# Kernel tuning notes

Measured on AMD Instinct MI355X. Metric: run time of the kernel, lower is better.

## Reference

```python
import jax, jax.numpy as jnp
import numpy as np


def setup_inputs() -> dict:
    key = jax.random.key(0)
    ks = jax.random.split(key, 8)
    B = 32768
    return {
        "x": jax.random.normal(ks[0], (B, 784), dtype=jnp.float32),
        "conv_w": jax.random.normal(ks[1], (3, 3), dtype=jnp.float32),
        "fc1_w": jax.random.normal(ks[2], (512, 676), dtype=jnp.float32) * 0.04,
        "fc1_b": jax.random.normal(ks[3], (512,), dtype=jnp.float32),
        "fc2_w": jax.random.normal(ks[4], (512, 512), dtype=jnp.float32) * 0.04,
        "fc2_b": jax.random.normal(ks[5], (512,), dtype=jnp.float32),
        "out_w": jax.random.normal(ks[6], (10, 512), dtype=jnp.float32) * 0.04,
        "out_b": jax.random.normal(ks[7], (10,), dtype=jnp.float32),
    }


def reference(x, conv_w, fc1_w, fc1_b, fc2_w, fc2_b, out_w, out_b):
    B = x.shape[0]
    img = x.reshape(B, 1, 28, 28)  # NCHW, single channel
    # Valid 3x3 cross-correlation (same math as the nested tensordot loop).
    kern = conv_w.reshape(1, 1, 3, 3)  # OIHW
    conv = jax.lax.conv_general_dilated(
        img, kern, window_strides=(1, 1), padding="VALID",
        dimension_numbers=("NCHW", "OIHW", "NCHW"))  # [B,1,26,26]
    h = conv.reshape(B, 26 * 26)
    h = jax.nn.relu(h @ fc1_w.T + fc1_b)
    h = jax.nn.relu(h @ fc2_w.T + fc2_b)
    return h @ out_w.T + out_b  # [B,10] logits
```

## Files before the change

kernel.cpp:

```cpp
#include <hip/hip_runtime.h>

typedef unsigned short ushort_t;
typedef __attribute__((ext_vector_type(8))) short bf16x8;
typedef __attribute__((ext_vector_type(4))) float f32x4;
typedef __attribute__((ext_vector_type(16))) float f32x16;

__device__ __forceinline__ unsigned short f2bf(float f) {
    union { float f; unsigned u; } v; v.f = f;
    unsigned r = v.u + 0x7FFFu + ((v.u >> 16) & 1u);
    return (unsigned short)(r >> 16);
}

__device__ __forceinline__ void gl_lds16(const void* g, void* l) {
    __builtin_amdgcn_global_load_lds(
        (const __attribute__((address_space(1))) unsigned int*)g,
        (__attribute__((address_space(3))) unsigned int*)l, 16, 0, 0);
}

__global__ __launch_bounds__(256) void prep_w(const float* __restrict__ fc1_w,
                                              const float* __restrict__ cw,
                                              const float* __restrict__ fc2_w,
                                              const float* __restrict__ out_w,
                                              ushort_t* __restrict__ W1,
                                              ushort_t* __restrict__ W2,
                                              ushort_t* __restrict__ W3) {
    const int idx = blockIdx.x * 256 + threadIdx.x;
    if (idx < 512 * 832) {
        int n = idx / 832, p = idx % 832;
        float acc = 0.f;
        if (p < 784) {
            int pr = p / 28, pc = p % 28;
#pragma unroll
            for (int dr = 0; dr < 3; ++dr) {
                int r = pr - dr;
                if (r < 0 || r >= 26) continue;
#pragma unroll
                for (int dc = 0; dc < 3; ++dc) {
                    int col = pc - dc;
                    if (col < 0 || col >= 26) continue;
                    acc += cw[dr * 3 + dc] * fc1_w[n * 676 + r * 26 + col];
                }
            }
        }
        W1[idx] = f2bf(acc);
    }
    if (idx < 512 * 512) W2[idx] = f2bf(fc2_w[idx]);
    if (idx < 16 * 512)  W3[idx] = (idx < 10 * 512) ? f2bf(out_w[idx]) : (ushort_t)0;
}

__global__ __launch_bounds__(512, 1) void mega(const float* __restrict__ x,
                                               const ushort_t* __restrict__ W1,
                                               const ushort_t* __restrict__ W2,
                                               const ushort_t* __restrict__ W3,
                                               const float* __restrict__ b1,
                                               const float* __restrict__ b2,
                                               const float* __restrict__ ob,
                                               float* __restrict__ out) {
    extern __shared__ ushort_t smem[];
    ushort_t* xs = smem;
    ushort_t* ws = smem + 4096;
    ushort_t* hs = smem + 4096 + 32768;

    const int tid = threadIdx.x;
    const int wave = tid >> 6, lane = tid & 63;
    const int m0 = blockIdx.x * 64;
    const int srow = lane >> 3, sseg = lane & 7, gseg = sseg ^ (srow & 7);
    const int r32 = lane & 31, half = lane >> 5;
    const int xrow = tid >> 3, xoct = tid & 7;

    f32x16 acc[2][2];
#pragma unroll
    for (int i = 0; i < 2; ++i)
#pragma unroll
        for (int j = 0; j < 2; ++j)
#pragma unroll
            for (int e = 0; e < 16; ++e) acc[i][j][e] = 0.f;

    for (int ks = 0; ks < 13; ++ks) {
        const int k0 = ks * 64;
#pragma unroll
        for (int t = 0; t < 8; ++t) {
            const int rb = wave * 64 + t * 8;
            gl_lds16(W1 + (size_t)(rb + srow) * 832 + k0 + gseg * 8, &ws[rb * 64]);
        }
        {
            const int gc = k0 + xoct * 8;
            bf16x8 xv;
            if (gc < 784) {
                const float* xp = &x[(size_t)(m0 + xrow) * 784 + gc];
                const float4 v0 = *(const float4*)xp;
                const float4 v1 = *(const float4*)(xp + 4);
                xv[0] = (short)f2bf(v0.x); xv[1] = (short)f2bf(v0.y);
                xv[2] = (short)f2bf(v0.z); xv[3] = (short)f2bf(v0.w);
                xv[4] = (short)f2bf(v1.x); xv[5] = (short)f2bf(v1.y);
                xv[6] = (short)f2bf(v1.z); xv[7] = (short)f2bf(v1.w);
            } else {
#pragma unroll
                for (int e = 0; e < 8; ++e) xv[e] = 0;
            }
            *(bf16x8*)&xs[xrow * 64 + ((xoct ^ (xrow & 7)) * 8)] = xv;
        }
        __syncthreads();
#pragma unroll
        for (int ksub = 0; ksub < 4; ++ksub) {
            const int q = 2 * ksub + half;
            bf16x8 af[2], bw[2];
#pragma unroll
            for (int i = 0; i < 2; ++i) {
                af[i] = *(const bf16x8*)&xs[(i * 32 + r32) * 64 + ((q ^ (r32 & 7)) * 8)];
                bw[i] = *(const bf16x8*)&ws[(wave * 64 + i * 32 + r32) * 64 + ((q ^ (r32 & 7)) * 8)];
            }
#pragma unroll
            for (int i = 0; i < 2; ++i)
#pragma unroll
                for (int j = 0; j < 2; ++j)
                    acc[i][j] = __builtin_amdgcn_mfma_f32_32x32x16_bf16(af[i], bw[j], acc[i][j], 0, 0, 0);
        }
        __syncthreads();
    }

#pragma unroll
    for (int j = 0; j < 2; ++j) {
        const int n = wave * 64 + j * 32 + r32;
        const float bb = b1[n];
        const int nseg = n >> 3, nrem = n & 7;
#pragma unroll
        for (int i = 0; i < 2; ++i) {
#pragma unroll
            for (int reg = 0; reg < 16; ++reg) {
                const int m = i * 32 + 4 * half + (reg & 3) + 8 * (reg >> 2);
                hs[m * 512 + ((nseg ^ (m & 7)) * 8) + nrem] = f2bf(fmaxf(acc[i][j][reg] + bb, 0.f));
            }
        }
    }
#pragma unroll
    for (int i = 0; i < 2; ++i)
#pragma unroll
        for (int j = 0; j < 2; ++j)
#pragma unroll
            for (int e = 0; e < 16; ++e) acc[i][j][e] = 0.f;
    __syncthreads();

    for (int ks = 0; ks < 8; ++ks) {
        const int k0 = ks * 64;
#pragma unroll
        for (int t = 0; t < 8; ++t) {
            const int rb = wave * 64 + t * 8;
            gl_lds16(W2 + (size_t)(rb + srow) * 512 + k0 + gseg * 8, &ws[rb * 64]);
        }
        __syncthreads();
#pragma unroll
        for (int ksub = 0; ksub < 4; ++ksub) {
            const int q = 2 * ksub + half;
            const int hq = 8 * ks + q;
            bf16x8 af[2], bw[2];
#pragma unroll
            for (int i = 0; i < 2; ++i) {
                const int m = i * 32 + r32;
                af[i] = *(const bf16x8*)&hs[m * 512 + ((hq ^ (m & 7)) * 8)];
                bw[i] = *(const bf16x8*)&ws[(wave * 64 + i * 32 + r32) * 64 + ((q ^ (r32 & 7)) * 8)];
            }
#pragma unroll
            for (int i = 0; i < 2; ++i)
#pragma unroll
                for (int j = 0; j < 2; ++j)
                    acc[i][j] = __builtin_amdgcn_mfma_f32_32x32x16_bf16(af[i], bw[j], acc[i][j], 0, 0, 0);
        }
        __syncthreads();
    }

#pragma unroll
    for (int j = 0; j < 2; ++j) {
        const int n = wave * 64 + j * 32 + r32;
        const float bb = b2[n];
        const int nseg = n >> 3, nrem = n & 7;
#pragma unroll
        for (int i = 0; i < 2; ++i) {
#pragma unroll
            for (int reg = 0; reg < 16; ++reg) {
                const int m = i * 32 + 4 * half + (reg & 3) + 8 * (reg >> 2);
                hs[m * 512 + ((nseg ^ (m & 7)) * 8) + nrem] = f2bf(fmaxf(acc[i][j][reg] + bb, 0.f));
            }
        }
    }
    __syncthreads();

    if (wave < 4) {
        const int quad = lane >> 4, l16 = lane & 15;
        const int row = wave * 16 + l16;
        f32x4 hacc = {0.f, 0.f, 0.f, 0.f};
#pragma unroll
        for (int ks = 0; ks < 16; ++ks) {
            const int seg = 4 * ks + quad;
            const bf16x8 a = *(const bf16x8*)&hs[row * 512 + ((seg ^ (row & 7)) * 8)];
            const bf16x8 b = *(const bf16x8*)&W3[l16 * 512 + ks * 32 + quad * 8];
            hacc = __builtin_amdgcn_mfma_f32_16x16x32_bf16(a, b, hacc, 0, 0, 0);
        }
        if (l16 < 10) {
            const float bb = ob[l16];
#pragma unroll
            for (int r = 0; r < 4; ++r)
                out[(size_t)(m0 + wave * 16 + quad * 4 + r) * 10 + l16] = hacc[r] + bb;
        }
    }
}

extern "C" void kernel_launch(void* const* d_in, const int* in_sizes, int n_in,
                              void* d_out, int out_size, void* d_ws, size_t ws_size,
                              hipStream_t stream) {
    const float* x      = (const float*)d_in[0];
    const float* conv_w = (const float*)d_in[1];
    const float* fc1_w  = (const float*)d_in[2];
    const float* fc1_b  = (const float*)d_in[3];
    const float* fc2_w  = (const float*)d_in[4];
    const float* fc2_b  = (const float*)d_in[5];
    const float* out_w  = (const float*)d_in[6];
    const float* out_b  = (const float*)d_in[7];
    float* out = (float*)d_out;

    ushort_t* W1 = (ushort_t*)d_ws;
    ushort_t* W2 = W1 + 512 * 832;
    ushort_t* W3 = W2 + 512 * 512;

    prep_w<<<dim3(1664), 256, 0, stream>>>(fc1_w, conv_w, fc2_w, out_w, W1, W2, W3);

    mega<<<dim3(512), 512, 139264, stream>>>(x, W1, W2, W3, fc1_b, fc2_b, out_b, out);
}
```

Measured before the change: 230.5 us.

## Double the row tile, read weights from global, and prefetch x into registers

Each block now handles 128 rows instead of 64, launching 256 blocks instead of 512, so every weight fragment is reused across twice as many rows. Weight fragments are read straight from global memory (relying on cache) instead of being staged into LDS, which removes the weight LDS buffer and the barriers around it. The x tile for the next k-step is prefetched into registers with nontemporal loads while the current step computes. The catch is the accumulator count: it doubles to 128 floats per thread, and launch_bounds(512,2) caps registers, which risks spilling. Also, the 147 KB LDS request may still allow only one block per CU.

```diff
diff --git a/kernel.cpp b/kernel.cpp
--- a/kernel.cpp
+++ b/kernel.cpp
@@ -9,12 +9,6 @@
     union { float f; unsigned u; } v; v.f = f;
     unsigned r = v.u + 0x7FFFu + ((v.u >> 16) & 1u);
     return (unsigned short)(r >> 16);
-}
-
-__device__ __forceinline__ void gl_lds16(const void* g, void* l) {
-    __builtin_amdgcn_global_load_lds(
-        (const __attribute__((address_space(1))) unsigned int*)g,
-        (__attribute__((address_space(3))) unsigned int*)l, 16, 0, 0);
 }
 
 __global__ __launch_bounds__(256) void prep_w(const float* __restrict__ fc1_w,
@@ -48,73 +42,85 @@
     if (idx < 16 * 512)  W3[idx] = (idx < 10 * 512) ? f2bf(out_w[idx]) : (ushort_t)0;
 }
 
-__global__ __launch_bounds__(512, 1) void mega(const float* __restrict__ x,
-                                               const ushort_t* __restrict__ W1,
-                                               const ushort_t* __restrict__ W2,
-                                               const ushort_t* __restrict__ W3,
-                                               const float* __restrict__ b1,
-                                               const float* __restrict__ b2,
-                                               const float* __restrict__ ob,
-                                               float* __restrict__ out) {
+__global__ __launch_bounds__(512, 2) void mega2(const float* __restrict__ x,
+                                                const ushort_t* __restrict__ W1,
+                                                const ushort_t* __restrict__ W2,
+                                                const ushort_t* __restrict__ W3,
+                                                const float* __restrict__ b1,
+                                                const float* __restrict__ b2,
+                                                const float* __restrict__ ob,
+                                                float* __restrict__ out) {
     extern __shared__ ushort_t smem[];
     ushort_t* xs = smem;
-    ushort_t* ws = smem + 4096;
-    ushort_t* hs = smem + 4096 + 32768;
+    ushort_t* hs = smem + 8192;
 
     const int tid = threadIdx.x;
     const int wave = tid >> 6, lane = tid & 63;
-    const int m0 = blockIdx.x * 64;
-    const int srow = lane >> 3, sseg = lane & 7, gseg = sseg ^ (srow & 7);
-    const int r32 = lane & 31, half = lane >> 5;
+    const int r32 = lane & 31, khalf = lane >> 5;
     const int xrow = tid >> 3, xoct = tid & 7;
-
-    f32x16 acc[2][2];
-#pragma unroll
-    for (int i = 0; i < 2; ++i)
-#pragma unroll
-        for (int j = 0; j < 2; ++j)
-#pragma unroll
-            for (int e = 0; e < 16; ++e) acc[i][j][e] = 0.f;
+    const int m0 = blockIdx.x * 128;
+
+    f32x16 acc[2][2][2];
+#pragma unroll
+    for (int a = 0; a < 2; ++a)
+#pragma unroll
+        for (int i = 0; i < 2; ++i)
+#pragma unroll
+            for (int j = 0; j < 2; ++j)
+#pragma unroll
+                for (int e = 0; e < 16; ++e) acc[a][i][j][e] = 0.f;
+
+    f32x4 xv0[2], xv1[2];
+    auto load_x = [&](int ks) {
+        const int gc = ks * 64 + xoct * 8;
+#pragma unroll
+        for (int mh = 0; mh < 2; ++mh) {
+            if (gc < 784) {
+                const f32x4* p = (const f32x4*)&x[(size_t)(m0 + mh * 64 + xrow) * 784 + gc];
+                xv0[mh] = __builtin_nontemporal_load(p);
+                xv1[mh] = __builtin_nontemporal_load(p + 1);
+            } else {
+                xv0[mh] = (f32x4){0.f, 0.f, 0.f, 0.f};
+                xv1[mh] = (f32x4){0.f, 0.f, 0.f, 0.f};
+            }
+        }
+    };
+    load_x(0);
 
     for (int ks = 0; ks < 13; ++ks) {
+#pragma unroll
+        for (int mh = 0; mh < 2; ++mh) {
+            bf16x8 xv;
+            xv[0] = (short)f2bf(xv0[mh].x); xv[1] = (short)f2bf(xv0[mh].y);
+            xv[2] = (short)f2bf(xv0[mh].z); xv[3] = (short)f2bf(xv0[mh].w);
+            xv[4] = (short)f2bf(xv1[mh].x); xv[5] = (short)f2bf(xv1[mh].y);
+            xv[6] = (short)f2bf(xv1[mh].z); xv[7] = (short)f2bf(xv1[mh].w);
+            *(bf16x8*)&xs[mh * 4096 + xrow * 64 + ((xoct ^ (xrow & 7)) * 8)] = xv;
+        }
+        __syncthreads();
+        if (ks < 12) load_x(ks + 1);
         const int k0 = ks * 64;
 #pragma unroll
-        for (int t = 0; t < 8; ++t) {
-            const int rb = wave * 64 + t * 8;
-            gl_lds16(W1 + (size_t)(rb + srow) * 832 + k0 + gseg * 8, &ws[rb * 64]);
-        }
-        {
-            const int gc = k0 + xoct * 8;
-            bf16x8 xv;
-            if (gc < 784) {
-                const float* xp = &x[(size_t)(m0 + xrow) * 784 + gc];
-                const float4 v0 = *(const float4*)xp;
-                const float4 v1 = *(const float4*)(xp + 4);
-                xv[0] = (short)f2bf(v0.x); xv[1] = (short)f2bf(v0.y);
-                xv[2] = (short)f2bf(v0.z); xv[3] = (short)f2bf(v0.w);
-                xv[4] = (short)f2bf(v1.x); xv[5] = (short)f2bf(v1.y);
-                xv[6] = (short)f2bf(v1.z); xv[7] = (short)f2bf(v1.w);
-            } else {
-#pragma unroll
-                for (int e = 0; e < 8; ++e) xv[e] = 0;
-            }
-            *(bf16x8*)&xs[xrow * 64 + ((xoct ^ (xrow & 7)) * 8)] = xv;
-        }
-        __syncthreads();
-#pragma unroll
         for (int ksub = 0; ksub < 4; ++ksub) {
-            const int q = 2 * ksub + half;
-            bf16x8 af[2], bw[2];
-#pragma unroll
-            for (int i = 0; i < 2; ++i) {
-                af[i] = *(const bf16x8*)&xs[(i * 32 + r32) * 64 + ((q ^ (r32 & 7)) * 8)];
-                bw[i] = *(const bf16x8*)&ws[(wave * 64 + i * 32 + r32) * 64 + ((q ^ (r32 & 7)) * 8)];
-            }
-#pragma unroll
-            for (int i = 0; i < 2; ++i)
-#pragma unroll
-                for (int j = 0; j < 2; ++j)
-                    acc[i][j] = __builtin_amdgcn_mfma_f32_32x32x16_bf16(af[i], bw[j], acc[i][j], 0, 0, 0);
+            const int q = 2 * ksub + khalf;
+            bf16x8 bw[2], af[2][2];
+#pragma unroll
+            for (int j = 0; j < 2; ++j)
+                bw[j] = *(const bf16x8*)&W1[(size_t)(wave * 64 + j * 32 + r32) * 832 + k0 + q * 8];
+#pragma unroll
+            for (int mh = 0; mh < 2; ++mh)
+#pragma unroll
+                for (int i = 0; i < 2; ++i) {
+                    const int mr = i * 32 + r32;
+                    af[mh][i] = *(const bf16x8*)&xs[mh * 4096 + mr * 64 + ((q ^ (mr & 7)) * 8)];
+                }
+#pragma unroll
+            for (int mh = 0; mh < 2; ++mh)
+#pragma unroll
+                for (int i = 0; i < 2; ++i)
+#pragma unroll
+                    for (int j = 0; j < 2; ++j)
+                        acc[mh][i][j] = __builtin_amdgcn_mfma_f32_32x32x16_bf16(af[mh][i], bw[j], acc[mh][i][j], 0, 0, 0);
         }
         __syncthreads();
     }
@@ -125,49 +131,52 @@
         const float bb = b1[n];
         const int nseg = n >> 3, nrem = n & 7;
 #pragma unroll
-        for (int i = 0; i < 2; ++i) {
-#pragma unroll
-            for (int reg = 0; reg < 16; ++reg) {
-                const int m = i * 32 + 4 * half + (reg & 3) + 8 * (reg >> 2);
-                hs[m * 512 + ((nseg ^ (m & 7)) * 8) + nrem] = f2bf(fmaxf(acc[i][j][reg] + bb, 0.f));
-            }
-        }
-    }
-#pragma unroll
-    for (int i = 0; i < 2; ++i)
-#pragma unroll
-        for (int j = 0; j < 2; ++j)
-#pragma unroll
-            for (int e = 0; e < 16; ++e) acc[i][j][e] = 0.f;
+        for (int mh = 0; mh < 2; ++mh)
+#pragma unroll
+            for (int i = 0; i < 2; ++i)
+#pragma unroll
+                for (int reg = 0; reg < 16; ++reg) {
+                    const int m = mh * 64 + i * 32 + 4 * khalf + (reg & 3) + 8 * (reg >> 2);
+                    hs[m * 512 + ((nseg ^ (m & 7)) * 8) + nrem] = f2bf(fmaxf(acc[mh][i][j][reg] + bb, 0.f));
+                }
+    }
+#pragma unroll
+    for (int a = 0; a < 2; ++a)
+#pragma unroll
+        for (int i = 0; i < 2; ++i)
+#pragma unroll
+            for (int j = 0; j < 2; ++j)
+#pragma unroll
+                for (int e = 0; e < 16; ++e) acc[a][i][j][e] = 0.f;
     __syncthreads();
 
     for (int ks = 0; ks < 8; ++ks) {
         const int k0 = ks * 64;
 #pragma unroll
-        for (int t = 0; t < 8; ++t) {
-            const int rb = wave * 64 + t * 8;
-            gl_lds16(W2 + (size_t)(rb + srow) * 512 + k0 + gseg * 8, &ws[rb * 64]);
-        }
-        __syncthreads();
-#pragma unroll
         for (int ksub = 0; ksub < 4; ++ksub) {
-            const int q = 2 * ksub + half;
-            const int hq = 8 * ks + q;
-            bf16x8 af[2], bw[2];
-#pragma unroll
-            for (int i = 0; i < 2; ++i) {
-                const int m = i * 32 + r32;
-                af[i] = *(const bf16x8*)&hs[m * 512 + ((hq ^ (m & 7)) * 8)];
-                bw[i] = *(const bf16x8*)&ws[(wave * 64 + i * 32 + r32) * 64 + ((q ^ (r32 & 7)) * 8)];
-            }
-#pragma unroll
-            for (int i = 0; i < 2; ++i)
-#pragma unroll
-                for (int j = 0; j < 2; ++j)
-                    acc[i][j] = __builtin_amdgcn_mfma_f32_32x32x16_bf16(af[i], bw[j], acc[i][j], 0, 0, 0);
-        }
-        __syncthreads();
-    }
+            const int q = 2 * ksub + khalf;
+            const int hq = ks * 8 + q;
+            bf16x8 bw[2], af[2][2];
+#pragma unroll
+            for (int j = 0; j < 2; ++j)
+                bw[j] = *(const bf16x8*)&W2[(size_t)(wave * 64 + j * 32 + r32) * 512 + k0 + q * 8];
+#pragma unroll
+            for (int mh = 0; mh < 2; ++mh)
+#pragma unroll
+                for (int i = 0; i < 2; ++i) {
+                    const int m = mh * 64 + i * 32 + r32;
+                    af[mh][i] = *(const bf16x8*)&hs[m * 512 + ((hq ^ (m & 7)) * 8)];
+                }
+#pragma unroll
+            for (int mh = 0; mh < 2; ++mh)
+#pragma unroll
+                for (int i = 0; i < 2; ++i)
+#pragma unroll
+                    for (int j = 0; j < 2; ++j)
+                        acc[mh][i][j] = __builtin_amdgcn_mfma_f32_32x32x16_bf16(af[mh][i], bw[j], acc[mh][i][j], 0, 0, 0);
+        }
+    }
+    __syncthreads();
 
 #pragma unroll
     for (int j = 0; j < 2; ++j) {
@@ -175,17 +184,18 @@
         const float bb = b2[n];
         const int nseg = n >> 3, nrem = n & 7;
 #pragma unroll
-        for (int i = 0; i < 2; ++i) {
-#pragma unroll
-            for (int reg = 0; reg < 16; ++reg) {
-                const int m = i * 32 + 4 * half + (reg & 3) + 8 * (reg >> 2);
-                hs[m * 512 + ((nseg ^ (m & 7)) * 8) + nrem] = f2bf(fmaxf(acc[i][j][reg] + bb, 0.f));
-            }
-        }
+        for (int mh = 0; mh < 2; ++mh)
+#pragma unroll
+            for (int i = 0; i < 2; ++i)
+#pragma unroll
+                for (int reg = 0; reg < 16; ++reg) {
+                    const int m = mh * 64 + i * 32 + 4 * khalf + (reg & 3) + 8 * (reg >> 2);
+                    hs[m * 512 + ((nseg ^ (m & 7)) * 8) + nrem] = f2bf(fmaxf(acc[mh][i][j][reg] + bb, 0.f));
+                }
     }
     __syncthreads();
 
-    if (wave < 4) {
+    {
         const int quad = lane >> 4, l16 = lane & 15;
         const int row = wave * 16 + l16;
         f32x4 hacc = {0.f, 0.f, 0.f, 0.f};
@@ -224,5 +234,5 @@
 
     prep_w<<<dim3(1664), 256, 0, stream>>>(fc1_w, conv_w, fc2_w, out_w, W1, W2, W3);
 
-    mega<<<dim3(512), 512, 139264, stream>>>(x, W1, W2, W3, fc1_b, fc2_b, out_b, out);
-}
+    mega2<<<dim3(256), 512, 147456, stream>>>(x, W1, W2, W3, fc1_b, fc2_b, out_b, out);
+}
```

Result: slower. 235.7 us (+2.3%).
